# Kernel optimization log

Measured on AMD Instinct MI355X. Metric: run time of the kernel, lower is better.

The kernel has to match this reference:

```python
import jax, jax.numpy as jnp
import numpy as np

D = 512
HEAD_NUMB = 8

def setup_inputs() -> dict:
    key = jax.random.key(0)
    k1, k2, k3 = jax.random.split(key, 3)
    x = jax.random.normal(k1, (4, 4096, D), dtype=jnp.float32)
    # nn.Linear(D, 3D): weight [3D, D], bias [3D]
    W_qkv = jax.random.normal(k2, (3 * D, D), dtype=jnp.float32) / np.sqrt(D)
    b_qkv = jax.random.normal(k3, (3 * D,), dtype=jnp.float32) * 0.01
    return {"x": x, "W_qkv": W_qkv, "b_qkv": b_qkv}

def reference(x, W_qkv, b_qkv):
    # fused QKV projection: x @ W^T + b  -> [B, N, 3D]
    qkv = jnp.einsum('bnd,ed->bne', x, W_qkv) + b_qkv
    q = qkv[:, :, :D]
    k = qkv[:, :, D:2 * D]
    v = qkv[:, :, 2 * D:]
    scaling = (D / HEAD_NUMB) ** (-0.5)
    # single-head attention over full D (faithful to the original module)
    scores = jnp.einsum('bqd,bkd->bqk', q, k) * scaling  # [B, N, N]
    attn = jax.nn.softmax(scores, axis=2)
    return jnp.einsum('bqk,bkd->bqd', attn, v)
```

## Files before the change

### kernel.cpp

```cpp
#include <hip/hip_runtime.h>
#include <hip/hip_bf16.h>

#define D_DIM 512
#define NSEQ  4096
#define BATCH 4
#define SCALE 0.125f

typedef __attribute__((ext_vector_type(8)))  short short8;
typedef __attribute__((ext_vector_type(16))) float floatx16;

__device__ __forceinline__ unsigned short f2bf(float f) {
    __hip_bfloat16 h = __float2bfloat16(f);
    return *reinterpret_cast<unsigned short*>(&h);
}

__device__ __forceinline__ floatx16 mfma_bf16(short8 a, short8 b, floatx16 c) {
    return __builtin_amdgcn_mfma_f32_32x32x16_bf16(a, b, c, 0, 0, 0);
}

#define K1_STRIDE 40

__global__ __launch_bounds__(256, 2) void qkv_gemm(
    const float* __restrict__ x, const float* __restrict__ W,
    const float* __restrict__ bias,
    unsigned short* __restrict__ qs, unsigned short* __restrict__ kk,
    unsigned short* __restrict__ vT)
{
    __shared__ __align__(16) unsigned short Xs[128 * K1_STRIDE];
    __shared__ __align__(16) unsigned short Ws[128 * K1_STRIDE];

    const int t = threadIdx.x;
    const int lane = t & 63, w = t >> 6;
    const int l31 = lane & 31, lh = lane >> 5;
    const int wm = w >> 1, we = w & 1;
    const int m0 = blockIdx.x * 128;
    const int n0 = blockIdx.y * 128;

    floatx16 a00, a01, a10, a11;
#pragma unroll
    for (int r = 0; r < 16; r++) { a00[r] = 0.f; a01[r] = 0.f; a10[r] = 0.f; a11[r] = 0.f; }

    for (int kc = 0; kc < 16; kc++) {
        const int k0 = kc * 32;
        __syncthreads();
#pragma unroll
        for (int p = 0; p < 4; p++) {
            int id = t + p * 256;
            int row = id >> 3, kq = id & 7;
            float4 xv = *(const float4*)(x + (size_t)(m0 + row) * D_DIM + k0 + 4 * kq);
            ushort4 hx; hx.x = f2bf(xv.x); hx.y = f2bf(xv.y); hx.z = f2bf(xv.z); hx.w = f2bf(xv.w);
            *(ushort4*)&Xs[row * K1_STRIDE + 4 * kq] = hx;
            float4 wv = *(const float4*)(W + (size_t)(n0 + row) * D_DIM + k0 + 4 * kq);
            ushort4 hw; hw.x = f2bf(wv.x); hw.y = f2bf(wv.y); hw.z = f2bf(wv.z); hw.w = f2bf(wv.w);
            *(ushort4*)&Ws[row * K1_STRIDE + 4 * kq] = hw;
        }
        __syncthreads();
#pragma unroll
        for (int ks = 0; ks < 2; ks++) {
            const int co = ks * 16 + lh * 8;
            short8 fa0 = *(const short8*)&Xs[(wm * 64 + l31) * K1_STRIDE + co];
            short8 fa1 = *(const short8*)&Xs[(wm * 64 + 32 + l31) * K1_STRIDE + co];
            short8 fb0 = *(const short8*)&Ws[(we * 64 + l31) * K1_STRIDE + co];
            short8 fb1 = *(const short8*)&Ws[(we * 64 + 32 + l31) * K1_STRIDE + co];
            a00 = mfma_bf16(fa0, fb0, a00);
            a01 = mfma_bf16(fa0, fb1, a01);
            a10 = mfma_bf16(fa1, fb0, a10);
            a11 = mfma_bf16(fa1, fb1, a11);
        }
    }

#pragma unroll
    for (int jt = 0; jt < 2; jt++) {
        const int e = n0 + we * 64 + jt * 32 + l31;
        const float bv = bias[e];
#pragma unroll
        for (int it = 0; it < 2; it++) {
            const int mb = m0 + wm * 64 + it * 32;
            const floatx16& av = (it == 0) ? ((jt == 0) ? a00 : a01)
                                           : ((jt == 0) ? a10 : a11);
            if (e < 512) {
#pragma unroll
                for (int r = 0; r < 16; r++) {
                    int m = mb + (r & 3) + 8 * (r >> 2) + 4 * lh;
                    qs[(size_t)m * D_DIM + e] = f2bf((av[r] + bv) * SCALE);
                }
            } else if (e < 1024) {
#pragma unroll
                for (int r = 0; r < 16; r++) {
                    int m = mb + (r & 3) + 8 * (r >> 2) + 4 * lh;
                    kk[(size_t)m * D_DIM + (e - 512)] = f2bf(av[r] + bv);
                }
            } else {
                const int d = e - 1024;
#pragma unroll
                for (int q = 0; q < 4; q++) {
                    int mq = mb + 8 * q + 4 * lh;
                    int bb = mq >> 12; int tok = mq & 4095;
                    ushort4 hv;
                    hv.x = f2bf(av[4 * q + 0] + bv); hv.y = f2bf(av[4 * q + 1] + bv);
                    hv.z = f2bf(av[4 * q + 2] + bv); hv.w = f2bf(av[4 * q + 3] + bv);
                    *(ushort4*)&vT[((size_t)bb * 512 + d) * 4096 + tok] = hv;
                }
            }
        }
    }
}

#define FA_BQ 64
#define FA_BK 256
#define FA_DC 128
#define QC_STR 136
#define KC_STR 136
#define P_STR  264
#define VT_STR 72

__global__ __launch_bounds__(512, 2) void flash_attn(
    const unsigned short* __restrict__ qs, const unsigned short* __restrict__ kk,
    const unsigned short* __restrict__ vT, float* __restrict__ out)
{
    __shared__ __align__(16) unsigned char smem[123392];
    unsigned short* Qc = (unsigned short*)(smem);
    unsigned short* Kc = (unsigned short*)(smem + 17408);
    unsigned short* Vt = (unsigned short*)(smem);
    unsigned short* P  = (unsigned short*)(smem + 87040);
    float* pmax    = (float*)(smem + 120832);
    float* psum    = (float*)(smem + 121856);
    float* alpha_s = (float*)(smem + 122880);
    float* l_s     = (float*)(smem + 123136);

    const int t = threadIdx.x;
    const int lane = t & 63, w = t >> 6;
    const int l31 = lane & 31, lh = lane >> 5;
    const int wi = w & 1, wjj = w >> 1;
    const int b  = blockIdx.y;
    const int q0 = blockIdx.x * FA_BQ;
    const size_t qbase = ((size_t)b * NSEQ + q0) * D_DIM;
    const size_t kbase = (size_t)b * NSEQ * D_DIM;
    const size_t vbase = (size_t)b * D_DIM * NSEQ;

    const int i_my = wi * 32 + l31;

    floatx16 o00, o01, o10, o11;
#pragma unroll
    for (int r = 0; r < 16; r++) { o00[r] = 0.f; o01[r] = 0.f; o10[r] = 0.f; o11[r] = 0.f; }
    float m_st = -__builtin_inff(), l_st = 0.f;

    for (int kt = 0; kt < NSEQ; kt += FA_BK) {
        floatx16 s0, s1;
#pragma unroll
        for (int r = 0; r < 16; r++) { s0[r] = 0.f; s1[r] = 0.f; }

        for (int dc = 0; dc < D_DIM; dc += FA_DC) {
            __syncthreads();
#pragma unroll
            for (int p = 0; p < 2; p++) {
                int id = t + p * 512;
                int row = id >> 4, c8 = id & 15;
                uint4 v = *(const uint4*)(qs + qbase + (size_t)row * D_DIM + dc + c8 * 8);
                *(uint4*)&Qc[row * QC_STR + c8 * 8] = v;
            }
#pragma unroll
            for (int p = 0; p < 8; p++) {
                int id = t + p * 512;
                int row = id >> 4, c8 = id & 15;
                uint4 v = *(const uint4*)(kk + kbase + (size_t)(kt + row) * D_DIM + dc + c8 * 8);
                *(uint4*)&Kc[row * KC_STR + c8 * 8] = v;
            }
            __syncthreads();
            const unsigned short* kr0 = &Kc[(wjj * 64 + l31) * KC_STR];
            const unsigned short* kr1 = kr0 + 32 * KC_STR;
            const unsigned short* qr  = &Qc[i_my * QC_STR];
#pragma unroll
            for (int ks = 0; ks < 8; ks++) {
                const int co = ks * 16 + lh * 8;
                short8 fa0 = *(const short8*)(kr0 + co);
                short8 fa1 = *(const short8*)(kr1 + co);
                short8 fb  = *(const short8*)(qr + co);
                s0 = mfma_bf16(fa0, fb, s0);
                s1 = mfma_bf16(fa1, fb, s1);
            }
        }

        float mx = -__builtin_inff();
#pragma unroll
        for (int r = 0; r < 16; r++) mx = fmaxf(mx, fmaxf(s0[r], s1[r]));
        mx = fmaxf(mx, __shfl_xor(mx, 32));
        if (lh == 0) pmax[i_my * 4 + wjj] = mx;
        __syncthreads();
        float4 pm = *(float4*)&pmax[i_my * 4];
        const float m_new = fmaxf(m_st, fmaxf(fmaxf(pm.x, pm.y), fmaxf(pm.z, pm.w)));
        const float alpha = __expf(m_st - m_new);
        m_st = m_new;

        float sum = 0.f;
        {
            const int prow = i_my * P_STR;
#pragma unroll
            for (int q = 0; q < 4; q++) {
                float p0 = __expf(s0[4*q+0] - m_new), p1 = __expf(s0[4*q+1] - m_new);
                float p2 = __expf(s0[4*q+2] - m_new), p3 = __expf(s0[4*q+3] - m_new);
                sum += (p0 + p1) + (p2 + p3);
                ushort4 h; h.x = f2bf(p0); h.y = f2bf(p1); h.z = f2bf(p2); h.w = f2bf(p3);
                *(ushort4*)&P[prow + (wjj*2+0)*32 + 8*q + 4*lh] = h;
            }
#pragma unroll
            for (int q = 0; q < 4; q++) {
                float p0 = __expf(s1[4*q+0] - m_new), p1 = __expf(s1[4*q+1] - m_new);
                float p2 = __expf(s1[4*q+2] - m_new), p3 = __expf(s1[4*q+3] - m_new);
                sum += (p0 + p1) + (p2 + p3);
                ushort4 h; h.x = f2bf(p0); h.y = f2bf(p1); h.z = f2bf(p2); h.w = f2bf(p3);
                *(ushort4*)&P[prow + (wjj*2+1)*32 + 8*q + 4*lh] = h;
            }
        }
        sum += __shfl_xor(sum, 32);
        if (lh == 0) psum[i_my * 4 + wjj] = sum;
        if (lh == 0 && wjj == 0) alpha_s[i_my] = alpha;
        __syncthreads();
        float4 ps = *(float4*)&psum[i_my * 4];
        l_st = l_st * alpha + ((ps.x + ps.y) + (ps.z + ps.w));

        float av[2][16];
        bool ch = false;
#pragma unroll
        for (int it = 0; it < 2; it++)
#pragma unroll
            for (int q = 0; q < 4; q++) {
                float4 a4 = *(float4*)&alpha_s[it * 32 + 8 * q + 4 * lh];
                av[it][4*q+0] = a4.x; av[it][4*q+1] = a4.y;
                av[it][4*q+2] = a4.z; av[it][4*q+3] = a4.w;
                ch = ch || (a4.x != 1.f) || (a4.y != 1.f) || (a4.z != 1.f) || (a4.w != 1.f);
            }
        if (__any(ch)) {
#pragma unroll
            for (int r = 0; r < 16; r++) {
                o00[r] *= av[0][r]; o01[r] *= av[0][r];
                o10[r] *= av[1][r]; o11[r] *= av[1][r];
            }
        }

        for (int jc = 0; jc < 4; jc++) {
            __syncthreads();
#pragma unroll
            for (int p = 0; p < 8; p++) {
                int id = t + p * 512;
                int d = id >> 3, c8 = id & 7;
                uint4 v = *(const uint4*)(vT + vbase + (size_t)d * NSEQ + kt + jc * 64 + c8 * 8);
                *(uint4*)&Vt[d * VT_STR + c8 * 8] = v;
            }
            __syncthreads();
            const unsigned short* pr0 = &P[l31 * P_STR + jc * 64];
            const unsigned short* pr1 = &P[(32 + l31) * P_STR + jc * 64];
            const unsigned short* vr0 = &Vt[(w * 64 + l31) * VT_STR];
            const unsigned short* vr1 = vr0 + 32 * VT_STR;
#pragma unroll
            for (int js = 0; js < 4; js++) {
                const int co = js * 16 + lh * 8;
                short8 pa0 = *(const short8*)(pr0 + co);
                short8 pa1 = *(const short8*)(pr1 + co);
                short8 vb0 = *(const short8*)(vr0 + co);
                short8 vb1 = *(const short8*)(vr1 + co);
                o00 = mfma_bf16(pa0, vb0, o00);
                o01 = mfma_bf16(pa0, vb1, o01);
                o10 = mfma_bf16(pa1, vb0, o10);
                o11 = mfma_bf16(pa1, vb1, o11);
            }
        }
    }

    if (lh == 0 && wjj == 0) l_s[i_my] = l_st;
    __syncthreads();
    float iv[2][16];
#pragma unroll
    for (int it = 0; it < 2; it++)
#pragma unroll
        for (int q = 0; q < 4; q++) {
            float4 l4 = *(float4*)&l_s[it * 32 + 8 * q + 4 * lh];
            iv[it][4*q+0] = 1.f / l4.x; iv[it][4*q+1] = 1.f / l4.y;
            iv[it][4*q+2] = 1.f / l4.z; iv[it][4*q+3] = 1.f / l4.w;
        }
#pragma unroll
    for (int it = 0; it < 2; it++) {
        const floatx16& oa = (it == 0) ? o00 : o10;
        const floatx16& ob = (it == 0) ? o01 : o11;
#pragma unroll
        for (int r = 0; r < 16; r++) {
            const int i = it * 32 + (r & 3) + 8 * (r >> 2) + 4 * lh;
            const size_t rowb = ((size_t)b * NSEQ + q0 + i) * D_DIM;
            out[rowb + w * 64 + l31]      = oa[r] * iv[it][r];
            out[rowb + w * 64 + 32 + l31] = ob[r] * iv[it][r];
        }
    }
}

extern "C" void kernel_launch(void* const* d_in, const int* in_sizes, int n_in,
                              void* d_out, int out_size, void* d_ws, size_t ws_size,
                              hipStream_t stream)
{
    (void)in_sizes; (void)n_in; (void)out_size; (void)ws_size;
    const float* x    = (const float*)d_in[0];
    const float* W    = (const float*)d_in[1];
    const float* bias = (const float*)d_in[2];
    float* out = (float*)d_out;

    unsigned short* qs = (unsigned short*)d_ws;
    unsigned short* kk = qs + (size_t)16384 * 512;
    unsigned short* vT = kk + (size_t)16384 * 512;

    qkv_gemm<<<dim3(128, 12), 256, 0, stream>>>(x, W, bias, qs, kk, vT);
    flash_attn<<<dim3(NSEQ / FA_BQ, BATCH), 512, 0, stream>>>(qs, kk, vT, out);
}
```

Before: 358.4 us.

## Stream K/V MFMA fragments straight from global and keep full Q in LDS

The attention kernel now loads the whole 64x512 Q tile into LDS once. K and V^T operand fragments are read directly from global memory into registers, replacing the per-chunk LDS staging loops and their many __syncthreads. Separately, the QKV GEMM doubles its K-step to 64 and raises launch_bounds occupancy to 3. This trades LDS traffic and barriers for strided global loads that depend on L1/L2 caching and on hiding memory latency.

```diff
diff --git a/kernel.cpp b/kernel.cpp
--- a/kernel.cpp
+++ b/kernel.cpp
@@ -18,9 +18,10 @@
     return __builtin_amdgcn_mfma_f32_32x32x16_bf16(a, b, c, 0, 0, 0);
 }
 
-#define K1_STRIDE 40
-
-__global__ __launch_bounds__(256, 2) void qkv_gemm(
+#define K1_BK 64
+#define K1_STRIDE 72
+
+__global__ __launch_bounds__(256, 3) void qkv_gemm(
     const float* __restrict__ x, const float* __restrict__ W,
     const float* __restrict__ bias,
     unsigned short* __restrict__ qs, unsigned short* __restrict__ kk,
@@ -40,13 +41,13 @@
 #pragma unroll
     for (int r = 0; r < 16; r++) { a00[r] = 0.f; a01[r] = 0.f; a10[r] = 0.f; a11[r] = 0.f; }
 
-    for (int kc = 0; kc < 16; kc++) {
-        const int k0 = kc * 32;
-        __syncthreads();
-#pragma unroll
-        for (int p = 0; p < 4; p++) {
+    for (int kc = 0; kc < D_DIM / K1_BK; kc++) {
+        const int k0 = kc * K1_BK;
+        __syncthreads();
+#pragma unroll
+        for (int p = 0; p < 8; p++) {
             int id = t + p * 256;
-            int row = id >> 3, kq = id & 7;
+            int row = id >> 4, kq = id & 15;
             float4 xv = *(const float4*)(x + (size_t)(m0 + row) * D_DIM + k0 + 4 * kq);
             ushort4 hx; hx.x = f2bf(xv.x); hx.y = f2bf(xv.y); hx.z = f2bf(xv.z); hx.w = f2bf(xv.w);
             *(ushort4*)&Xs[row * K1_STRIDE + 4 * kq] = hx;
@@ -56,7 +57,7 @@
         }
         __syncthreads();
 #pragma unroll
-        for (int ks = 0; ks < 2; ks++) {
+        for (int ks = 0; ks < 4; ks++) {
             const int co = ks * 16 + lh * 8;
             short8 fa0 = *(const short8*)&Xs[(wm * 64 + l31) * K1_STRIDE + co];
             short8 fa1 = *(const short8*)&Xs[(wm * 64 + 32 + l31) * K1_STRIDE + co];
@@ -108,25 +109,20 @@
 
 #define FA_BQ 64
 #define FA_BK 256
-#define FA_DC 128
-#define QC_STR 136
-#define KC_STR 136
-#define P_STR  264
-#define VT_STR 72
+#define Q_STR 520
+#define P_STR 264
 
 __global__ __launch_bounds__(512, 2) void flash_attn(
     const unsigned short* __restrict__ qs, const unsigned short* __restrict__ kk,
     const unsigned short* __restrict__ vT, float* __restrict__ out)
 {
-    __shared__ __align__(16) unsigned char smem[123392];
-    unsigned short* Qc = (unsigned short*)(smem);
-    unsigned short* Kc = (unsigned short*)(smem + 17408);
-    unsigned short* Vt = (unsigned short*)(smem);
-    unsigned short* P  = (unsigned short*)(smem + 87040);
-    float* pmax    = (float*)(smem + 120832);
-    float* psum    = (float*)(smem + 121856);
-    float* alpha_s = (float*)(smem + 122880);
-    float* l_s     = (float*)(smem + 123136);
+    __shared__ __align__(16) unsigned char smem[102912];
+    unsigned short* Qs = (unsigned short*)(smem);
+    unsigned short* P  = (unsigned short*)(smem + 66560);
+    float* pmax    = (float*)(smem + 100352);
+    float* psum    = (float*)(smem + 101376);
+    float* alpha_s = (float*)(smem + 102400);
+    float* l_s     = (float*)(smem + 102656);
 
     const int t = threadIdx.x;
     const int lane = t & 63, w = t >> 6;
@@ -140,45 +136,41 @@
 
     const int i_my = wi * 32 + l31;
 
+#pragma unroll
+    for (int p = 0; p < 8; p++) {
+        int id = t + p * 512;
+        int row = id >> 6, c8 = id & 63;
+        uint4 v = *(const uint4*)(qs + qbase + (size_t)row * D_DIM + c8 * 8);
+        *(uint4*)&Qs[row * Q_STR + c8 * 8] = v;
+    }
+    if (t < FA_BQ) {  }
+    __syncthreads();
+
+    const unsigned short* vp0 = vT + vbase + (size_t)(w * 64 + l31) * NSEQ;
+    const unsigned short* vp1 = vp0 + (size_t)32 * NSEQ;
+    const unsigned short* qrow = &Qs[i_my * Q_STR];
+
     floatx16 o00, o01, o10, o11;
 #pragma unroll
     for (int r = 0; r < 16; r++) { o00[r] = 0.f; o01[r] = 0.f; o10[r] = 0.f; o11[r] = 0.f; }
     float m_st = -__builtin_inff(), l_st = 0.f;
 
     for (int kt = 0; kt < NSEQ; kt += FA_BK) {
+        const unsigned short* kp0 = kk + kbase + (size_t)(kt + wjj * 64 + l31) * D_DIM;
+        const unsigned short* kp1 = kp0 + (size_t)32 * D_DIM;
+
         floatx16 s0, s1;
 #pragma unroll
         for (int r = 0; r < 16; r++) { s0[r] = 0.f; s1[r] = 0.f; }
 
-        for (int dc = 0; dc < D_DIM; dc += FA_DC) {
-            __syncthreads();
-#pragma unroll
-            for (int p = 0; p < 2; p++) {
-                int id = t + p * 512;
-                int row = id >> 4, c8 = id & 15;
-                uint4 v = *(const uint4*)(qs + qbase + (size_t)row * D_DIM + dc + c8 * 8);
-                *(uint4*)&Qc[row * QC_STR + c8 * 8] = v;
-            }
-#pragma unroll
-            for (int p = 0; p < 8; p++) {
-                int id = t + p * 512;
-                int row = id >> 4, c8 = id & 15;
-                uint4 v = *(const uint4*)(kk + kbase + (size_t)(kt + row) * D_DIM + dc + c8 * 8);
-                *(uint4*)&Kc[row * KC_STR + c8 * 8] = v;
-            }
-            __syncthreads();
-            const unsigned short* kr0 = &Kc[(wjj * 64 + l31) * KC_STR];
-            const unsigned short* kr1 = kr0 + 32 * KC_STR;
-            const unsigned short* qr  = &Qc[i_my * QC_STR];
-#pragma unroll
-            for (int ks = 0; ks < 8; ks++) {
-                const int co = ks * 16 + lh * 8;
-                short8 fa0 = *(const short8*)(kr0 + co);
-                short8 fa1 = *(const short8*)(kr1 + co);
-                short8 fb  = *(const short8*)(qr + co);
-                s0 = mfma_bf16(fa0, fb, s0);
-                s1 = mfma_bf16(fa1, fb, s1);
-            }
+#pragma unroll 8
+        for (int ks = 0; ks < 32; ks++) {
+            const int co = ks * 16 + lh * 8;
+            short8 fa0 = *(const short8*)(kp0 + co);
+            short8 fa1 = *(const short8*)(kp1 + co);
+            short8 fb  = *(const short8*)(qrow + co);
+            s0 = mfma_bf16(fa0, fb, s0);
+            s1 = mfma_bf16(fa1, fb, s1);
         }
 
         float mx = -__builtin_inff();
@@ -187,6 +179,7 @@
         mx = fmaxf(mx, __shfl_xor(mx, 32));
         if (lh == 0) pmax[i_my * 4 + wjj] = mx;
         __syncthreads();
+
         float4 pm = *(float4*)&pmax[i_my * 4];
         const float m_new = fmaxf(m_st, fmaxf(fmaxf(pm.x, pm.y), fmaxf(pm.z, pm.w)));
         const float alpha = __expf(m_st - m_new);
@@ -194,14 +187,14 @@
 
         float sum = 0.f;
         {
-            const int prow = i_my * P_STR;
+            const int prow = i_my * P_STR + wjj * 64;
 #pragma unroll
             for (int q = 0; q < 4; q++) {
                 float p0 = __expf(s0[4*q+0] - m_new), p1 = __expf(s0[4*q+1] - m_new);
                 float p2 = __expf(s0[4*q+2] - m_new), p3 = __expf(s0[4*q+3] - m_new);
                 sum += (p0 + p1) + (p2 + p3);
                 ushort4 h; h.x = f2bf(p0); h.y = f2bf(p1); h.z = f2bf(p2); h.w = f2bf(p3);
-                *(ushort4*)&P[prow + (wjj*2+0)*32 + 8*q + 4*lh] = h;
+                *(ushort4*)&P[prow + 8 * q + 4 * lh] = h;
             }
 #pragma unroll
             for (int q = 0; q < 4; q++) {
@@ -209,13 +202,14 @@
                 float p2 = __expf(s1[4*q+2] - m_new), p3 = __expf(s1[4*q+3] - m_new);
                 sum += (p0 + p1) + (p2 + p3);
                 ushort4 h; h.x = f2bf(p0); h.y = f2bf(p1); h.z = f2bf(p2); h.w = f2bf(p3);
-                *(ushort4*)&P[prow + (wjj*2+1)*32 + 8*q + 4*lh] = h;
+                *(ushort4*)&P[prow + 32 + 8 * q + 4 * lh] = h;
             }
         }
         sum += __shfl_xor(sum, 32);
         if (lh == 0) psum[i_my * 4 + wjj] = sum;
         if (lh == 0 && wjj == 0) alpha_s[i_my] = alpha;
         __syncthreads();
+
         float4 ps = *(float4*)&psum[i_my * 4];
         l_st = l_st * alpha + ((ps.x + ps.y) + (ps.z + ps.w));
 
@@ -238,32 +232,19 @@
             }
         }
 
-        for (int jc = 0; jc < 4; jc++) {
-            __syncthreads();
-#pragma unroll
-            for (int p = 0; p < 8; p++) {
-                int id = t + p * 512;
-                int d = id >> 3, c8 = id & 7;
-                uint4 v = *(const uint4*)(vT + vbase + (size_t)d * NSEQ + kt + jc * 64 + c8 * 8);
-                *(uint4*)&Vt[d * VT_STR + c8 * 8] = v;
-            }
-            __syncthreads();
-            const unsigned short* pr0 = &P[l31 * P_STR + jc * 64];
-            const unsigned short* pr1 = &P[(32 + l31) * P_STR + jc * 64];
-            const unsigned short* vr0 = &Vt[(w * 64 + l31) * VT_STR];
-            const unsigned short* vr1 = vr0 + 32 * VT_STR;
-#pragma unroll
-            for (int js = 0; js < 4; js++) {
-                const int co = js * 16 + lh * 8;
-                short8 pa0 = *(const short8*)(pr0 + co);
-                short8 pa1 = *(const short8*)(pr1 + co);
-                short8 vb0 = *(const short8*)(vr0 + co);
-                short8 vb1 = *(const short8*)(vr1 + co);
-                o00 = mfma_bf16(pa0, vb0, o00);
-                o01 = mfma_bf16(pa0, vb1, o01);
-                o10 = mfma_bf16(pa1, vb0, o10);
-                o11 = mfma_bf16(pa1, vb1, o11);
-            }
+        const unsigned short* vq0 = vp0 + kt;
+        const unsigned short* vq1 = vp1 + kt;
+#pragma unroll 4
+        for (int ks = 0; ks < 16; ks++) {
+            const int co = ks * 16 + lh * 8;
+            short8 pa0 = *(const short8*)&P[l31 * P_STR + co];
+            short8 pa1 = *(const short8*)&P[(32 + l31) * P_STR + co];
+            short8 vb0 = *(const short8*)(vq0 + co);
+            short8 vb1 = *(const short8*)(vq1 + co);
+            o00 = mfma_bf16(pa0, vb0, o00);
+            o01 = mfma_bf16(pa0, vb1, o01);
+            o10 = mfma_bf16(pa1, vb0, o10);
+            o11 = mfma_bf16(pa1, vb1, o11);
         }
     }
 
```

New measurement: 511.4 us. +42.7%, slower.
